# Kernel tuning notes

Hardware: AMD Instinct MI355X
Metric: run time of the kernel (lower is better)

Reference implementation:

```python
import jax, jax.numpy as jnp
import numpy as np

DN = ('NCHW', 'OIHW', 'NCHW')
B, H, W = 2048, 16, 16
DICT, SE, CE, ESZ, NZ = 14, 8, 16, 512, 512
EPS = 1e-4


def _conv(x, w, b):
    # 3x3 conv, padding=1 (SAME), NCHW
    return jax.lax.conv_general_dilated(x, w, (1, 1), 'SAME', dimension_numbers=DN) + b[None, :, None, None]


def _normalized(m, eps=0.0):
    return m / (jnp.sqrt(jnp.sum(m * m, axis=1, keepdims=True)) + eps)


def setup_inputs() -> dict:
    key = jax.random.key(0)
    ks = jax.random.split(key, 20)
    f = jnp.float32
    d = {
        's': jax.random.randint(ks[0], (B, H, W), 0, DICT, dtype=jnp.int32),
        's_prime': jax.random.randint(ks[1], (B, H, W), 0, DICT, dtype=jnp.int32),
        'state_embed': jax.random.normal(ks[2], (DICT, SE), f),
        'conv_embed_w': jax.random.normal(ks[3], (CE, SE, 3, 3), f) * 0.1,
        'conv_embed_b': jnp.zeros((CE,), f),
        'p1c1_w': jax.random.normal(ks[4], (16, CE, 3, 3), f) * 0.1,
        'p1c1_b': jnp.zeros((16,), f),
        'p1c2_w': jax.random.normal(ks[5], (32, 16, 3, 3), f) * 0.1,
        'p1c2_b': jnp.zeros((32,), f),
        'p1l_w': jax.random.normal(ks[6], (ESZ, 32 * H * W), f) * 0.02,
        'p1l_b': jnp.zeros((ESZ,), f),
        'p2c1_w': jax.random.normal(ks[7], (16, CE, 3, 3), f) * 0.1,
        'p2c1_b': jnp.zeros((16,), f),
        'p2c2_w': jax.random.normal(ks[8], (32, 16, 3, 3), f) * 0.1,
        'p2c2_b': jnp.zeros((32,), f),
        'p2l_w': jax.random.normal(ks[9], (ESZ, 32 * H * W), f) * 0.02,
        'p2l_b': jnp.zeros((ESZ,), f),
        'z_vectors': jax.random.normal(ks[10], (NZ, ESZ), f),
        'scale': jnp.ones((1,), f),
        'downscale_factor': 1,
    }
    return d


def _embed(s, state_embed, conv_embed_w, conv_embed_b):
    # nn.Embedding(max_norm=1): renorm rows to L2 norm <= 1 before lookup
    norms = jnp.sqrt(jnp.sum(state_embed * state_embed, axis=1, keepdims=True))
    table = state_embed / jnp.maximum(norms, 1.0)
    x = table[s]  # (B, H, W, SE)
    x = jnp.transpose(x, (0, 3, 1, 2))  # (B, SE, H, W)
    return _conv(x, conv_embed_w, conv_embed_b)


def _tower(x, c1w, c1b, c2w, c2b, lw, lb):
    x = jax.nn.relu(_conv(x, c1w, c1b))
    x = jax.nn.relu(_conv(x, c2w, c2b))
    x = x.reshape(x.shape[0], -1)  # (B, 32*H*W)
    x = x @ lw.T + lb
    return _normalized(x, EPS)


def reference(s, s_prime, state_embed, conv_embed_w, conv_embed_b,
              p1c1_w, p1c1_b, p1c2_w, p1c2_b, p1l_w, p1l_b,
              p2c1_w, p2c1_b, p2c2_w, p2c2_b, p2l_w, p2l_b,
              z_vectors, scale, downscale_factor):
    s_e = _embed(s, state_embed, conv_embed_w, conv_embed_b)
    sp_e = _embed(s_prime, state_embed, conv_embed_w, conv_embed_b)
    embed1 = _tower(s_e, p1c1_w, p1c1_b, p1c2_w, p1c2_b, p1l_w, p1l_b)
    embed2 = _tower(sp_e - s_e, p2c1_w, p2c1_b, p2c2_w, p2c2_b, p2l_w, p2l_b)
    # VQ: cosine-similarity nearest codebook vector
    zn = _normalized(z_vectors, 0.0)  # (NZ, ESZ)
    z_inds = jnp.argmax(embed2 @ zn.T, axis=1)  # (B,)
    z_matrix = zn[z_inds]  # (B, ESZ)
    if downscale_factor == 1:
        ipm = embed1 @ z_matrix.T  # (B, B)
    else:
        bs = embed1.shape[0] // downscale_factor
        v1 = embed1[::downscale_factor]  # (bs, ESZ)
        v2 = z_matrix.reshape(bs, downscale_factor, -1)
        ipm = jnp.einsum('be,bde->bd', v1, v2)
    return jnp.exp(scale) * ipm
```

## Files before the change

### kernel.cpp

```cpp
#include <hip/hip_runtime.h>
#include <math.h>


typedef __attribute__((ext_vector_type(8))) __bf16 bf16x8;
typedef __attribute__((ext_vector_type(4))) float f32x4;
typedef __attribute__((ext_vector_type(8))) unsigned short ushort8;
typedef __attribute__((ext_vector_type(4))) unsigned short ushort4v;

static __device__ __forceinline__ unsigned short f2bf(float x) {
  union { float f; unsigned u; } v; v.f = x;
  return (unsigned short)(v.u >> 16);
}
static __device__ __forceinline__ float bf2f(unsigned short h) {
  union { float f; unsigned u; } v; v.u = ((unsigned)h) << 16;
  return v.f;
}
template<int NS>
static __device__ __forceinline__ void split3(float x, unsigned short* h) {
  unsigned short q0 = f2bf(x); h[0] = q0;
  float r1 = x - bf2f(q0);
  unsigned short q1 = f2bf(r1); h[1] = q1;
  if constexpr (NS == 3) h[2] = f2bf(r1 - bf2f(q1));
}
static __device__ __forceinline__ void gload_lds16(const void* g, void* l) {
  __builtin_amdgcn_global_load_lds(
      (const __attribute__((address_space(1))) unsigned int*)g,
      (__attribute__((address_space(3))) unsigned int*)l, 16, 0, 0);
}
#define MFMA16(a, b, c) __builtin_amdgcn_mfma_f32_16x16x32_bf16((a), (b), (c), 0, 0, 0)

template<int NS>
static __device__ __forceinline__ f32x4 mfma_prod(const bf16x8* a, const bf16x8* b, f32x4 c) {
  c = MFMA16(a[0], b[0], c);
  c = MFMA16(a[0], b[1], c);
  c = MFMA16(a[1], b[0], c);
  if constexpr (NS == 3) {
    c = MFMA16(a[1], b[1], c);
    c = MFMA16(a[0], b[2], c);
    c = MFMA16(a[2], b[0], c);
  }
  return c;
}
static __device__ __forceinline__ int conv_a16(int cell, int half) {
  return (cell * 2 + half) ^ ((cell >> 2) & 7);
}

__global__ __launch_bounds__(128) void prep_table_kernel(
    const float* __restrict__ se, float* __restrict__ tbl)
{
  int t = threadIdx.x;
  if (t < 112) {
    int r = t >> 3;
    float ss = 0.f;
    #pragma unroll
    for (int i = 0; i < 8; ++i) { float v = se[r * 8 + i]; ss += v * v; }
    float n = fmaxf(sqrtf(ss), 1.0f);
    tbl[t] = se[t] / n;
  }
}

__global__ __launch_bounds__(256) void reduce_norm_kernel(
    const float* __restrict__ pre, const float* __restrict__ bias, float eps,
    unsigned short* __restrict__ o0, unsigned short* __restrict__ o1,
    unsigned short* __restrict__ o2)
{
  int row = blockIdx.x, t = threadIdx.x;
  size_t base = (size_t)row * 512 + t * 2;
  float2 v = *reinterpret_cast<const float2*>(pre + base);
  float ax = v.x, ay = v.y;
  if (bias) { ax += bias[t * 2]; ay += bias[t * 2 + 1]; }
  float ss = ax * ax + ay * ay;
  #pragma unroll
  for (int m = 32; m >= 1; m >>= 1) ss += __shfl_xor(ss, m, 64);
  __shared__ float wsum[4];
  int lane = t & 63, wid = t >> 6;
  if (lane == 0) wsum[wid] = ss;
  __syncthreads();
  float tot = wsum[0] + wsum[1] + wsum[2] + wsum[3];
  float inv = 1.0f / (sqrtf(tot) + eps);
  float a = ax * inv, b = ay * inv;
  unsigned short ha[3], hb[3];
  split3<3>(a, ha); split3<3>(b, hb);
  o0[base] = ha[0]; o0[base + 1] = hb[0];
  o1[base] = ha[1]; o1[base + 1] = hb[1];
  if (o2) { o2[base] = ha[2]; o2[base + 1] = hb[2]; }
}

__global__ __launch_bounds__(256) void prep_wt_kernel(
    const float* __restrict__ src, unsigned short* __restrict__ dst,
    int NSs, int OC, int mode)
{
  int total = 3 * NSs * 4 * OC * 8;
  int i = blockIdx.x * 256 + threadIdx.x;
  if (i >= total) return;
  int ic = i & 7;
  int r = i >> 3;
  int oc = r % OC; r /= OC;
  int kc = r & 3; r >>= 2;
  int s = r % NSs;
  int sp = r / NSs;
  int tap, icf, IC;
  if (mode == 0) { tap = s * 4 + kc; icf = ic; IC = 8; }
  else           { tap = s * 2 + (kc >> 1); icf = (kc & 1) * 8 + ic; IC = 16; }
  float w = 0.f;
  if (tap < 9) {
    int ky = tap / 3, kx = tap - ky * 3;
    w = src[((oc * IC + icf) * 3 + ky) * 3 + kx];
  }
  unsigned short h[3];
  split3<3>(w, h);
  dst[i] = h[sp];
}

template<int NS>
__global__ __launch_bounds__(256) void tower_mfma_kernel(
    const int* __restrict__ sIdx, const int* __restrict__ spIdx,
    const float* __restrict__ tblf,
    const unsigned short* __restrict__ wtE,
    const unsigned short* __restrict__ wt1,
    const unsigned short* __restrict__ wt2,
    const float* __restrict__ eb, const float* __restrict__ c1b,
    const float* __restrict__ c2b,
    unsigned short* __restrict__ a0, unsigned short* __restrict__ a1,
    unsigned short* __restrict__ a2, int delta)
{
  __shared__ float tbl[112];
  __shared__ ushort8 G[NS][324];
  __shared__ ushort8 Abuf[NS][648];
  __shared__ ushort8 Bbuf[NS][648];

  const int b = blockIdx.x, t = threadIdx.x;
  const int lane = t & 63, wv = t >> 6;
  const int fr = lane & 15, kc = lane >> 4;

  if (t < 112) tbl[t] = tblf[t];
  {
    int4 zz = {0, 0, 0, 0};
    int4* gz = (int4*)G;
    for (int i = t; i < NS * 324; i += 256) gz[i] = zz;
    int4* az = (int4*)Abuf;
    for (int i = t; i < NS * 648; i += 256) az[i] = zz;
    int4* bz = (int4*)Bbuf;
    for (int i = t; i < NS * 648; i += 256) bz[i] = zz;
  }
  __syncthreads();

  {
    const int y = t >> 4, x = t & 15;
    const int cell = (y + 1) * 18 + (x + 1);
    int sv = sIdx[(size_t)b * 256 + t];
    float v[8];
    if (delta) {
      int spv = spIdx[(size_t)b * 256 + t];
      #pragma unroll
      for (int c = 0; c < 8; ++c) v[c] = tbl[spv * 8 + c] - tbl[sv * 8 + c];
    } else {
      #pragma unroll
      for (int c = 0; c < 8; ++c) v[c] = tbl[sv * 8 + c];
    }
    ushort8 h0, h1, h2;
    #pragma unroll
    for (int c = 0; c < 8; ++c) {
      unsigned short q[3];
      split3<NS>(v[c], q);
      h0[c] = q[0]; h1[c] = q[1];
      if constexpr (NS == 3) h2[c] = q[2];
    }
    G[0][cell] = h0; G[1][cell] = h1;
    if constexpr (NS == 3) G[2][cell] = h2;
  }
  __syncthreads();

  {
    float bias = 0.f;
    if (!delta) bias = eb[fr];
    f32x4 acc[4];
    #pragma unroll
    for (int j = 0; j < 4; ++j) acc[j] = (f32x4)0.f;
    #pragma unroll
    for (int s = 0; s < 3; ++s) {
      bf16x8 bw[NS];
      #pragma unroll
      for (int sp = 0; sp < NS; ++sp)
        bw[sp] = __builtin_bit_cast(bf16x8, *reinterpret_cast<const ushort8*>(
            wtE + (size_t)(((sp * 3 + s) * 4 + kc) * 16 + fr) * 8));
      int tap = s * 4 + kc; if (tap > 8) tap = 8;
      const int dy = tap / 3, dx = tap - dy * 3;
      const int cb = dy * 18 + fr + dx;
      #pragma unroll
      for (int j = 0; j < 4; ++j) {
        const int cell = cb + (wv * 4 + j) * 18;
        bf16x8 av[NS];
        #pragma unroll
        for (int sp = 0; sp < NS; ++sp)
          av[sp] = __builtin_bit_cast(bf16x8, G[sp][cell]);
        acc[j] = mfma_prod<NS>(av, bw, acc[j]);
      }
    }
    #pragma unroll
    for (int j = 0; j < 4; ++j) {
      const int y = wv * 4 + j;
      #pragma unroll
      for (int q = 0; q < 4; ++q) {
        const int x = kc * 4 + q;
        const int cell = (y + 1) * 18 + (x + 1);
        const int a16 = conv_a16(cell, fr >> 3);
        unsigned short hh[3];
        split3<NS>(acc[j][q] + bias, hh);
        #pragma unroll
        for (int sp = 0; sp < NS; ++sp)
          ((unsigned short*)&Abuf[sp][0])[a16 * 8 + (fr & 7)] = hh[sp];
      }
    }
  }
  __syncthreads();

  {
    const float bias = c1b[fr];
    f32x4 acc[4];
    #pragma unroll
    for (int j = 0; j < 4; ++j) acc[j] = (f32x4)0.f;
    #pragma unroll
    for (int s = 0; s < 5; ++s) {
      bf16x8 bw[NS];
      #pragma unroll
      for (int sp = 0; sp < NS; ++sp)
        bw[sp] = __builtin_bit_cast(bf16x8, *reinterpret_cast<const ushort8*>(
            wt1 + (size_t)(((sp * 5 + s) * 4 + kc) * 16 + fr) * 8));
      int tap = s * 2 + (kc >> 1); if (tap > 8) tap = 8;
      const int dy = tap / 3, dx = tap - dy * 3;
      const int half = kc & 1;
      const int cb = dy * 18 + fr + dx;
      #pragma unroll
      for (int j = 0; j < 4; ++j) {
        const int cell = cb + (wv * 4 + j) * 18;
        const int a16 = conv_a16(cell, half);
        bf16x8 av[NS];
        #pragma unroll
        for (int sp = 0; sp < NS; ++sp)
          av[sp] = __builtin_bit_cast(bf16x8, *reinterpret_cast<const ushort8*>(
              (const unsigned short*)&Abuf[sp][0] + a16 * 8));
        acc[j] = mfma_prod<NS>(av, bw, acc[j]);
      }
    }
    #pragma unroll
    for (int j = 0; j < 4; ++j) {
      const int y = wv * 4 + j;
      #pragma unroll
      for (int q = 0; q < 4; ++q) {
        const int x = kc * 4 + q;
        const int cell = (y + 1) * 18 + (x + 1);
        const int a16 = conv_a16(cell, fr >> 3);
        unsigned short hh[3];
        split3<NS>(fmaxf(acc[j][q] + bias, 0.f), hh);
        #pragma unroll
        for (int sp = 0; sp < NS; ++sp)
          ((unsigned short*)&Bbuf[sp][0])[a16 * 8 + (fr & 7)] = hh[sp];
      }
    }
  }
  __syncthreads();

  {
    const float bias0 = c2b[fr], bias1 = c2b[16 + fr];
    f32x4 acc0[4], acc1[4];
    #pragma unroll
    for (int j = 0; j < 4; ++j) { acc0[j] = (f32x4)0.f; acc1[j] = (f32x4)0.f; }
    #pragma unroll
    for (int s = 0; s < 5; ++s) {
      bf16x8 bw0[NS], bw1[NS];
      #pragma unroll
      for (int sp = 0; sp < NS; ++sp) {
        size_t base = (size_t)(((sp * 5 + s) * 4 + kc) * 32) * 8;
        bw0[sp] = __builtin_bit_cast(bf16x8,
            *reinterpret_cast<const ushort8*>(wt2 + base + (size_t)fr * 8));
        bw1[sp] = __builtin_bit_cast(bf16x8,
            *reinterpret_cast<const ushort8*>(wt2 + base + (size_t)(16 + fr) * 8));
      }
      int tap = s * 2 + (kc >> 1); if (tap > 8) tap = 8;
      const int dy = tap / 3, dx = tap - dy * 3;
      const int half = kc & 1;
      const int cb = dy * 18 + fr + dx;
      #pragma unroll
      for (int j = 0; j < 4; ++j) {
        const int cell = cb + (wv * 4 + j) * 18;
        const int a16 = conv_a16(cell, half);
        bf16x8 av[NS];
        #pragma unroll
        for (int sp = 0; sp < NS; ++sp)
          av[sp] = __builtin_bit_cast(bf16x8, *reinterpret_cast<const ushort8*>(
              (const unsigned short*)&Bbuf[sp][0] + a16 * 8));
        acc0[j] = mfma_prod<NS>(av, bw0, acc0[j]);
        acc1[j] = mfma_prod<NS>(av, bw1, acc1[j]);
      }
    }
    #pragma unroll
    for (int j = 0; j < 4; ++j) {
      const int y = wv * 4 + j;
      ushort4v g0[2], g1[2], g2[2];
      #pragma unroll
      for (int q = 0; q < 4; ++q) {
        unsigned short hh[3];
        split3<NS>(fmaxf(acc0[j][q] + bias0, 0.f), hh);
        g0[0][q] = hh[0]; g1[0][q] = hh[1]; if constexpr (NS == 3) g2[0][q] = hh[2];
        split3<NS>(fmaxf(acc1[j][q] + bias1, 0.f), hh);
        g0[1][q] = hh[0]; g1[1][q] = hh[1]; if constexpr (NS == 3) g2[1][q] = hh[2];
      }
      size_t base0 = (size_t)b * 8192 + (size_t)fr * 256 + y * 16 + kc * 4;
      size_t base1 = base0 + 16 * 256;
      *reinterpret_cast<ushort4v*>(a0 + base0) = g0[0];
      *reinterpret_cast<ushort4v*>(a0 + base1) = g0[1];
      *reinterpret_cast<ushort4v*>(a1 + base0) = g1[0];
      *reinterpret_cast<ushort4v*>(a1 + base1) = g1[1];
      if constexpr (NS == 3) {
        *reinterpret_cast<ushort4v*>(a2 + base0) = g2[0];
        *reinterpret_cast<ushort4v*>(a2 + base1) = g2[1];
      }
    }
  }
}

template<int NS, bool BF32, bool GATHER, bool ATOMIC, bool FINAL>
__global__ __launch_bounds__(256) void mfma_gemm_kernel(
    const unsigned short* __restrict__ A0, const unsigned short* __restrict__ A1,
    const unsigned short* __restrict__ A2,
    const unsigned short* __restrict__ B0, const unsigned short* __restrict__ B1,
    const unsigned short* __restrict__ B2,
    const float* __restrict__ Bf32,
    const int* __restrict__ gather, const float* __restrict__ scale_p,
    float* __restrict__ C, int M, int N, int K, int Ksub)
{
  __shared__ unsigned short ldsA[NS][4096];
  __shared__ unsigned short ldsB[NS][4096];

  const int t = threadIdx.x;
  const int lane = t & 63, wv = t >> 6;
  const int m0 = blockIdx.x * 128, n0 = blockIdx.y * 128;
  const long kbase = (long)blockIdx.z * Ksub;
  const int NT = Ksub >> 5;

  const int st_row = lane >> 2;
  const int st_cb = (lane & 3) * 16;
  int srow[2];
  long bgrow[2];
  #pragma unroll
  for (int r = 0; r < 2; ++r) {
    srow[r] = (wv + 4 * r) * 16 + st_row;
    if constexpr (!BF32) {
      long g = n0 + srow[r];
      if constexpr (GATHER) g = gather[n0 + srow[r]];
      bgrow[r] = g;
    }
  }

  const int wr = wv >> 1, wc = wv & 1;
  const int fr = lane & 15, kc = lane >> 4;

  f32x4 acc[4][4];
  #pragma unroll
  for (int mi = 0; mi < 4; ++mi)
    #pragma unroll
    for (int ni = 0; ni < 4; ++ni) acc[mi][ni] = (f32x4)0.f;

  const unsigned short* Asp[3] = {A0, A1, A2};
  const unsigned short* Bsp[3] = {B0, B1, B2};

  for (int kt = 0; kt < NT; ++kt) {
    const long k0 = kbase + (long)kt * 32;
    #pragma unroll
    for (int sp = 0; sp < NS; ++sp)
      #pragma unroll
      for (int r = 0; r < 2; ++r) {
        int row = srow[r];
        int c = st_cb ^ (((row >> 1) & 3) << 4);
        gload_lds16(Asp[sp] + (size_t)(m0 + row) * K + k0 + (c >> 1),
                    &ldsA[sp][(wv + 4 * r) * 512]);
      }
    if constexpr (BF32) {
      #pragma unroll
      for (int i = 0; i < 4; ++i) {
        int row = (t >> 3) + 32 * i;
        f32x4 v = *reinterpret_cast<const f32x4*>(
            Bf32 + (size_t)(n0 + row) * K + k0 + (t & 7) * 4);
        int cb = ((t & 7) * 8) ^ (((row >> 1) & 3) << 4);
        ushort4v w0, w1, w2;
        #pragma unroll
        for (int jj = 0; jj < 4; ++jj) {
          unsigned short hh[3];
          split3<NS>(v[jj], hh);
          w0[jj] = hh[0]; w1[jj] = hh[1];
          if constexpr (NS == 3) w2[jj] = hh[2];
        }
        *reinterpret_cast<ushort4v*>(&ldsB[0][row * 32 + (cb >> 1)]) = w0;
        *reinterpret_cast<ushort4v*>(&ldsB[1][row * 32 + (cb >> 1)]) = w1;
        if constexpr (NS == 3)
          *reinterpret_cast<ushort4v*>(&ldsB[2][row * 32 + (cb >> 1)]) = w2;
      }
    } else {
      #pragma unroll
      for (int sp = 0; sp < NS; ++sp)
        #pragma unroll
        for (int r = 0; r < 2; ++r) {
          int row = srow[r];
          int c = st_cb ^ (((row >> 1) & 3) << 4);
          gload_lds16(Bsp[sp] + (size_t)bgrow[r] * K + k0 + (c >> 1),
                      &ldsB[sp][(wv + 4 * r) * 512]);
        }
    }
    __syncthreads();

    bf16x8 af[NS][4], bf[NS][4];
    #pragma unroll
    for (int sp = 0; sp < NS; ++sp) {
      #pragma unroll
      for (int mi = 0; mi < 4; ++mi) {
        int row = wr * 64 + mi * 16 + fr;
        int cb = (kc * 16) ^ (((row >> 1) & 3) << 4);
        af[sp][mi] = __builtin_bit_cast(bf16x8,
            *reinterpret_cast<const ushort8*>(&ldsA[sp][row * 32 + (cb >> 1)]));
      }
      #pragma unroll
      for (int ni = 0; ni < 4; ++ni) {
        int row = wc * 64 + ni * 16 + fr;
        int cb = (kc * 16) ^ (((row >> 1) & 3) << 4);
        bf[sp][ni] = __builtin_bit_cast(bf16x8,
            *reinterpret_cast<const ushort8*>(&ldsB[sp][row * 32 + (cb >> 1)]));
      }
    }
    #pragma unroll
    for (int mi = 0; mi < 4; ++mi)
      #pragma unroll
      for (int ni = 0; ni < 4; ++ni) {
        f32x4 c = acc[mi][ni];
        c = MFMA16(af[0][mi], bf[0][ni], c);
        c = MFMA16(af[0][mi], bf[1][ni], c);
        c = MFMA16(af[1][mi], bf[0][ni], c);
        if constexpr (NS == 3) {
          c = MFMA16(af[1][mi], bf[1][ni], c);
          c = MFMA16(af[0][mi], bf[2][ni], c);
          c = MFMA16(af[2][mi], bf[0][ni], c);
        }
        acc[mi][ni] = c;
      }
    __syncthreads();
  }

  if constexpr (ATOMIC) {
    #pragma unroll
    for (int mi = 0; mi < 4; ++mi)
      #pragma unroll
      for (int ni = 0; ni < 4; ++ni) {
        int col = n0 + wc * 64 + ni * 16 + fr;
        #pragma unroll
        for (int q = 0; q < 4; ++q) {
          int row = m0 + wr * 64 + mi * 16 + kc * 4 + q;
          atomicAdd(&C[(size_t)row * N + col], acc[mi][ni][q]);
        }
      }
  } else {
    float scl = 1.0f;
    if constexpr (FINAL) scl = expf(scale_p[0]);
    #pragma unroll
    for (int mi = 0; mi < 4; ++mi)
      #pragma unroll
      for (int ni = 0; ni < 4; ++ni) {
        int col = n0 + wc * 64 + ni * 16 + fr;
        #pragma unroll
        for (int q = 0; q < 4; ++q) {
          int row = m0 + wr * 64 + mi * 16 + kc * 4 + q;
          C[(size_t)row * N + col] = acc[mi][ni][q] * scl;
        }
      }
  }
}

__global__ __launch_bounds__(256) void argmax_rows_kernel(
    const float* __restrict__ S, int* __restrict__ inds)
{
  __shared__ float vals[256];
  __shared__ int idxs[256];
  int row = blockIdx.x, t = threadIdx.x;
  float best = -INFINITY; int bi = 1 << 30;
  #pragma unroll
  for (int r = 0; r < 2; ++r) {
    int j = t + r * 256;
    float v = S[(size_t)row * 512 + j];
    if (v > best) { best = v; bi = j; }
  }
  vals[t] = best; idxs[t] = bi;
  __syncthreads();
  for (int off = 128; off > 0; off >>= 1) {
    if (t < off) {
      float v2 = vals[t + off]; int i2 = idxs[t + off];
      if (v2 > vals[t] || (v2 == vals[t] && i2 < idxs[t])) {
        vals[t] = v2; idxs[t] = i2;
      }
    }
    __syncthreads();
  }
  if (t == 0) inds[row] = idxs[0];
}

extern "C" void kernel_launch(void* const* d_in, const int* in_sizes, int n_in,
                              void* d_out, int out_size, void* d_ws, size_t ws_size,
                              hipStream_t stream)
{
  const int*   s      = (const int*)  d_in[0];
  const int*   sprime = (const int*)  d_in[1];
  const float* se     = (const float*)d_in[2];
  const float* ew     = (const float*)d_in[3];
  const float* eb     = (const float*)d_in[4];
  const float* p1c1w  = (const float*)d_in[5];
  const float* p1c1b  = (const float*)d_in[6];
  const float* p1c2w  = (const float*)d_in[7];
  const float* p1c2b  = (const float*)d_in[8];
  const float* p1lw   = (const float*)d_in[9];
  const float* p1lb   = (const float*)d_in[10];
  const float* p2c1w  = (const float*)d_in[11];
  const float* p2c1b  = (const float*)d_in[12];
  const float* p2c2w  = (const float*)d_in[13];
  const float* p2c2b  = (const float*)d_in[14];
  const float* p2lw   = (const float*)d_in[15];
  const float* p2lb   = (const float*)d_in[16];
  const float* zv     = (const float*)d_in[17];
  const float* scale  = (const float*)d_in[18];
  float* out = (float*)d_out;

  char* w = (char*)d_ws;
  size_t off = 0;
  auto alloc = [&](size_t bytes) -> char* {
    char* p = w + off;
    off += (bytes + 255) & ~(size_t)255;
    return p;
  };
  float* tblf = (float*)alloc(112 * 4);
  unsigned short* zn0 = (unsigned short*)alloc((size_t)512 * 512 * 2);
  unsigned short* zn1 = (unsigned short*)alloc((size_t)512 * 512 * 2);
  unsigned short* zn2 = (unsigned short*)alloc((size_t)512 * 512 * 2);
  unsigned short* e10 = (unsigned short*)alloc((size_t)2048 * 512 * 2);
  unsigned short* e11 = (unsigned short*)alloc((size_t)2048 * 512 * 2);
  unsigned short* e20 = (unsigned short*)alloc((size_t)2048 * 512 * 2);
  unsigned short* e21 = (unsigned short*)alloc((size_t)2048 * 512 * 2);
  unsigned short* e22 = (unsigned short*)alloc((size_t)2048 * 512 * 2);
  float* epre = (float*)alloc((size_t)2048 * 512 * 4);
  float* sc   = epre;
  int*   zi   = (int*)alloc(2048 * 4);
  unsigned short* wtE  = (unsigned short*)alloc(4608 * 2);
  unsigned short* wt1a = (unsigned short*)alloc(7680 * 2);
  unsigned short* wt2a = (unsigned short*)alloc(15360 * 2);
  unsigned short* wt1b = (unsigned short*)alloc(7680 * 2);
  unsigned short* wt2b = (unsigned short*)alloc(15360 * 2);
  unsigned short* act0 = (unsigned short*)alloc((size_t)2048 * 8192 * 2);
  unsigned short* act1 = (unsigned short*)alloc((size_t)2048 * 8192 * 2);
  unsigned short* act2 = (unsigned short*)alloc((size_t)2048 * 8192 * 2);

  prep_table_kernel<<<1, 128, 0, stream>>>(se, tblf);
  reduce_norm_kernel<<<512, 256, 0, stream>>>(zv, nullptr, 0.0f, zn0, zn1, zn2);
  prep_wt_kernel<<<18, 256, 0, stream>>>(ew,    wtE,  3, 16, 0);
  prep_wt_kernel<<<30, 256, 0, stream>>>(p1c1w, wt1a, 5, 16, 1);
  prep_wt_kernel<<<60, 256, 0, stream>>>(p1c2w, wt2a, 5, 32, 1);
  prep_wt_kernel<<<30, 256, 0, stream>>>(p2c1w, wt1b, 5, 16, 1);
  prep_wt_kernel<<<60, 256, 0, stream>>>(p2c2w, wt2b, 5, 32, 1);

  tower_mfma_kernel<2><<<2048, 256, 0, stream>>>(
      s, sprime, tblf, wtE, wt1a, wt2a, eb, p1c1b, p1c2b, act0, act1, act2, 0);
  hipMemsetAsync(epre, 0, (size_t)2048 * 512 * 4, stream);
  mfma_gemm_kernel<2, true, false, true, false><<<dim3(16, 4, 8), 256, 0, stream>>>(
      act0, act1, nullptr, nullptr, nullptr, nullptr, p1lw, nullptr, nullptr,
      epre, 2048, 512, 8192, 1024);
  reduce_norm_kernel<<<2048, 256, 0, stream>>>(epre, p1lb, 1e-4f, e10, e11, nullptr);

  tower_mfma_kernel<3><<<2048, 256, 0, stream>>>(
      s, sprime, tblf, wtE, wt1b, wt2b, eb, p2c1b, p2c2b, act0, act1, act2, 1);
  hipMemsetAsync(epre, 0, (size_t)2048 * 512 * 4, stream);
  mfma_gemm_kernel<3, true, false, true, false><<<dim3(16, 4, 8), 256, 0, stream>>>(
      act0, act1, act2, nullptr, nullptr, nullptr, p2lw, nullptr, nullptr,
      epre, 2048, 512, 8192, 1024);
  reduce_norm_kernel<<<2048, 256, 0, stream>>>(epre, p2lb, 1e-4f, e20, e21, e22);

  mfma_gemm_kernel<3, false, false, false, false><<<dim3(16, 4, 1), 256, 0, stream>>>(
      e20, e21, e22, zn0, zn1, zn2, nullptr, nullptr, nullptr,
      sc, 2048, 512, 512, 512);
  argmax_rows_kernel<<<2048, 256, 0, stream>>>(sc, zi);
  mfma_gemm_kernel<2, false, true, false, true><<<dim3(16, 16, 1), 256, 0, stream>>>(
      e10, e11, nullptr, zn0, zn1, nullptr, nullptr, zi, scale,
      out, 2048, 2048, 512, 512);
}
```

Measured before the change: 486.4 us.

## Fuse argmax into score GEMM, merge prep kernels, trim halo zeroing, deepen split-K

New measurement: 502.7 us. 1.03x slower.

```diff
diff --git a/kernel.cpp b/kernel.cpp
--- a/kernel.cpp
+++ b/kernel.cpp
@@ -44,55 +44,79 @@
 static __device__ __forceinline__ int conv_a16(int cell, int half) {
   return (cell * 2 + half) ^ ((cell >> 2) & 7);
 }
-
-__global__ __launch_bounds__(128) void prep_table_kernel(
-    const float* __restrict__ se, float* __restrict__ tbl)
+static __device__ __forceinline__ unsigned long long score_key(float v, int col) {
+  unsigned b = __float_as_uint(v);
+  unsigned m = b ^ ((unsigned)((int)b >> 31) | 0x80000000u);
+  return ((unsigned long long)m << 32) | (unsigned)(511 - col);
+}
+static __device__ __forceinline__ unsigned long long shfl_xor_u64(unsigned long long v, int m) {
+  unsigned lo = __shfl_xor((unsigned)v, m, 64);
+  unsigned hi = __shfl_xor((unsigned)(v >> 32), m, 64);
+  return ((unsigned long long)hi << 32) | lo;
+}
+
+__global__ __launch_bounds__(256) void prep_misc_kernel(
+    const float* __restrict__ se, float* __restrict__ tbl,
+    const float* __restrict__ zv,
+    unsigned short* __restrict__ zn0, unsigned short* __restrict__ zn1,
+    unsigned short* __restrict__ zn2,
+    float* __restrict__ epre, unsigned long long* __restrict__ zi)
 {
-  int t = threadIdx.x;
-  if (t < 112) {
-    int r = t >> 3;
-    float ss = 0.f;
-    #pragma unroll
-    for (int i = 0; i < 8; ++i) { float v = se[r * 8 + i]; ss += v * v; }
-    float n = fmaxf(sqrtf(ss), 1.0f);
-    tbl[t] = se[t] / n;
-  }
-}
-
-__global__ __launch_bounds__(256) void reduce_norm_kernel(
-    const float* __restrict__ pre, const float* __restrict__ bias, float eps,
-    unsigned short* __restrict__ o0, unsigned short* __restrict__ o1,
-    unsigned short* __restrict__ o2)
+  __shared__ float wsum[4];
+  const int b = blockIdx.x, t = threadIdx.x;
+  if (b == 0) {
+    if (t < 112) {
+      int r = t >> 3;
+      float ss = 0.f;
+      #pragma unroll
+      for (int i = 0; i < 8; ++i) { float v = se[r * 8 + i]; ss += v * v; }
+      float n = fmaxf(sqrtf(ss), 1.0f);
+      tbl[t] = se[t] / n;
+    }
+  } else if (b <= 512) {
+    int row = b - 1;
+    size_t base = (size_t)row * 512 + t * 2;
+    float2 v = *reinterpret_cast<const float2*>(zv + base);
+    float ss = v.x * v.x + v.y * v.y;
+    #pragma unroll
+    for (int m = 32; m >= 1; m >>= 1) ss += __shfl_xor(ss, m, 64);
+    int lane = t & 63, wid = t >> 6;
+    if (lane == 0) wsum[wid] = ss;
+    __syncthreads();
+    float tot = wsum[0] + wsum[1] + wsum[2] + wsum[3];
+    float inv = 1.0f / sqrtf(tot);
+    float a = v.x * inv, c = v.y * inv;
+    unsigned short ha[3], hc[3];
+    split3<3>(a, ha); split3<3>(c, hc);
+    zn0[base] = ha[0]; zn0[base + 1] = hc[0];
+    zn1[base] = ha[1]; zn1[base + 1] = hc[1];
+    zn2[base] = ha[2]; zn2[base + 1] = hc[2];
+  } else if (b <= 1024) {
+    f32x4 z4 = {0.f, 0.f, 0.f, 0.f};
+    size_t o = ((size_t)(b - 513) * 256 + t) * 8;
+    *reinterpret_cast<f32x4*>(epre + o) = z4;
+    *reinterpret_cast<f32x4*>(epre + o + 4) = z4;
+  } else {
+    int i = (b - 1025) * 256 + t;
+    if (i < 2048) zi[i] = 0ull;
+  }
+}
+
+__global__ __launch_bounds__(256) void prep_wt_all_kernel(
+    const float* __restrict__ ew,
+    const float* __restrict__ p1c1w, const float* __restrict__ p1c2w,
+    const float* __restrict__ p2c1w, const float* __restrict__ p2c2w,
+    unsigned short* __restrict__ wt)
 {
-  int row = blockIdx.x, t = threadIdx.x;
-  size_t base = (size_t)row * 512 + t * 2;
-  float2 v = *reinterpret_cast<const float2*>(pre + base);
-  float ax = v.x, ay = v.y;
-  if (bias) { ax += bias[t * 2]; ay += bias[t * 2 + 1]; }
-  float ss = ax * ax + ay * ay;
-  #pragma unroll
-  for (int m = 32; m >= 1; m >>= 1) ss += __shfl_xor(ss, m, 64);
-  __shared__ float wsum[4];
-  int lane = t & 63, wid = t >> 6;
-  if (lane == 0) wsum[wid] = ss;
-  __syncthreads();
-  float tot = wsum[0] + wsum[1] + wsum[2] + wsum[3];
-  float inv = 1.0f / (sqrtf(tot) + eps);
-  float a = ax * inv, b = ay * inv;
-  unsigned short ha[3], hb[3];
-  split3<3>(a, ha); split3<3>(b, hb);
-  o0[base] = ha[0]; o0[base + 1] = hb[0];
-  o1[base] = ha[1]; o1[base + 1] = hb[1];
-  if (o2) { o2[base] = ha[2]; o2[base + 1] = hb[2]; }
-}
-
-__global__ __launch_bounds__(256) void prep_wt_kernel(
-    const float* __restrict__ src, unsigned short* __restrict__ dst,
-    int NSs, int OC, int mode)
-{
-  int total = 3 * NSs * 4 * OC * 8;
-  int i = blockIdx.x * 256 + threadIdx.x;
-  if (i >= total) return;
+  int gi = blockIdx.x * 256 + threadIdx.x;
+  if (gi >= 50688) return;
+  const float* src; int off, NSs, OC, mode;
+  if (gi < 4608)       { src = ew;    off = 0;     NSs = 3; OC = 16; mode = 0; }
+  else if (gi < 12288) { src = p1c1w; off = 4608;  NSs = 5; OC = 16; mode = 1; }
+  else if (gi < 27648) { src = p1c2w; off = 12288; NSs = 5; OC = 32; mode = 1; }
+  else if (gi < 35328) { src = p2c1w; off = 27648; NSs = 5; OC = 16; mode = 1; }
+  else                 { src = p2c2w; off = 35328; NSs = 5; OC = 32; mode = 1; }
+  int i = gi - off;
   int ic = i & 7;
   int r = i >> 3;
   int oc = r % OC; r /= OC;
@@ -109,7 +133,37 @@
   }
   unsigned short h[3];
   split3<3>(w, h);
-  dst[i] = h[sp];
+  wt[gi] = h[sp];
+}
+
+__global__ __launch_bounds__(256) void reduce_norm_kernel(
+    const float* __restrict__ pre, const float* __restrict__ bias, float eps,
+    unsigned short* __restrict__ o0, unsigned short* __restrict__ o1,
+    unsigned short* __restrict__ o2, float* __restrict__ zero_dst)
+{
+  int row = blockIdx.x, t = threadIdx.x;
+  size_t base = (size_t)row * 512 + t * 2;
+  float2 v = *reinterpret_cast<const float2*>(pre + base);
+  float ax = v.x + bias[t * 2], ay = v.y + bias[t * 2 + 1];
+  float ss = ax * ax + ay * ay;
+  #pragma unroll
+  for (int m = 32; m >= 1; m >>= 1) ss += __shfl_xor(ss, m, 64);
+  __shared__ float wsum[4];
+  int lane = t & 63, wid = t >> 6;
+  if (lane == 0) wsum[wid] = ss;
+  __syncthreads();
+  float tot = wsum[0] + wsum[1] + wsum[2] + wsum[3];
+  float inv = 1.0f / (sqrtf(tot) + eps);
+  float a = ax * inv, b2 = ay * inv;
+  unsigned short ha[3], hb[3];
+  split3<3>(a, ha); split3<3>(b2, hb);
+  o0[base] = ha[0]; o0[base + 1] = hb[0];
+  o1[base] = ha[1]; o1[base + 1] = hb[1];
+  if (o2) { o2[base] = ha[2]; o2[base + 1] = hb[2]; }
+  if (zero_dst) {
+    float2 z = {0.f, 0.f};
+    *reinterpret_cast<float2*>(zero_dst + base) = z;
+  }
 }
 
 template<int NS>
@@ -134,14 +188,21 @@
   const int fr = lane & 15, kc = lane >> 4;
 
   if (t < 112) tbl[t] = tblf[t];
-  {
-    int4 zz = {0, 0, 0, 0};
-    int4* gz = (int4*)G;
-    for (int i = t; i < NS * 324; i += 256) gz[i] = zz;
-    int4* az = (int4*)Abuf;
-    for (int i = t; i < NS * 648; i += 256) az[i] = zz;
-    int4* bz = (int4*)Bbuf;
-    for (int i = t; i < NS * 648; i += 256) bz[i] = zz;
+  if (t < 68) {
+    int c;
+    if (t < 18)      c = t;
+    else if (t < 36) c = 306 + (t - 18);
+    else if (t < 52) c = 18 * (t - 35);
+    else             c = 18 * (t - 51) + 17;
+    ushort8 z8 = {0, 0, 0, 0, 0, 0, 0, 0};
+    #pragma unroll
+    for (int sp = 0; sp < NS; ++sp) {
+      G[sp][c] = z8;
+      ((ushort8*)&Abuf[sp][0])[conv_a16(c, 0)] = z8;
+      ((ushort8*)&Abuf[sp][0])[conv_a16(c, 1)] = z8;
+      ((ushort8*)&Bbuf[sp][0])[conv_a16(c, 0)] = z8;
+      ((ushort8*)&Bbuf[sp][0])[conv_a16(c, 1)] = z8;
+    }
   }
   __syncthreads();
 
@@ -320,14 +381,16 @@
   }
 }
 
-template<int NS, bool BF32, bool GATHER, bool ATOMIC, bool FINAL>
+template<int NS, bool BF32, int EPI>
 __global__ __launch_bounds__(256) void mfma_gemm_kernel(
     const unsigned short* __restrict__ A0, const unsigned short* __restrict__ A1,
     const unsigned short* __restrict__ A2,
     const unsigned short* __restrict__ B0, const unsigned short* __restrict__ B1,
     const unsigned short* __restrict__ B2,
     const float* __restrict__ Bf32,
-    const int* __restrict__ gather, const float* __restrict__ scale_p,
+    const unsigned long long* __restrict__ gkey,
+    unsigned long long* __restrict__ zout,
+    const float* __restrict__ scale_p,
     float* __restrict__ C, int M, int N, int K, int Ksub)
 {
   __shared__ unsigned short ldsA[NS][4096];
@@ -348,7 +411,8 @@
     srow[r] = (wv + 4 * r) * 16 + st_row;
     if constexpr (!BF32) {
       long g = n0 + srow[r];
-      if constexpr (GATHER) g = gather[n0 + srow[r]];
+      if constexpr (EPI == 2)
+        g = 511 - (long)(unsigned)(gkey[n0 + srow[r]] & 0xFFFFFFFFull);
       bgrow[r] = g;
     }
   }
@@ -445,7 +509,7 @@
     __syncthreads();
   }
 
-  if constexpr (ATOMIC) {
+  if constexpr (EPI == 0) {
     #pragma unroll
     for (int mi = 0; mi < 4; ++mi)
       #pragma unroll
@@ -457,9 +521,8 @@
           atomicAdd(&C[(size_t)row * N + col], acc[mi][ni][q]);
         }
       }
-  } else {
-    float scl = 1.0f;
-    if constexpr (FINAL) scl = expf(scale_p[0]);
+  } else if constexpr (EPI == 2) {
+    float scl = expf(scale_p[0]);
     #pragma unroll
     for (int mi = 0; mi < 4; ++mi)
       #pragma unroll
@@ -471,34 +534,27 @@
           C[(size_t)row * N + col] = acc[mi][ni][q] * scl;
         }
       }
-  }
-}
-
-__global__ __launch_bounds__(256) void argmax_rows_kernel(
-    const float* __restrict__ S, int* __restrict__ inds)
-{
-  __shared__ float vals[256];
-  __shared__ int idxs[256];
-  int row = blockIdx.x, t = threadIdx.x;
-  float best = -INFINITY; int bi = 1 << 30;
-  #pragma unroll
-  for (int r = 0; r < 2; ++r) {
-    int j = t + r * 256;
-    float v = S[(size_t)row * 512 + j];
-    if (v > best) { best = v; bi = j; }
-  }
-  vals[t] = best; idxs[t] = bi;
-  __syncthreads();
-  for (int off = 128; off > 0; off >>= 1) {
-    if (t < off) {
-      float v2 = vals[t + off]; int i2 = idxs[t + off];
-      if (v2 > vals[t] || (v2 == vals[t] && i2 < idxs[t])) {
-        vals[t] = v2; idxs[t] = i2;
-      }
-    }
-    __syncthreads();
-  }
-  if (t == 0) inds[row] = idxs[0];
+  } else {
+    #pragma unroll
+    for (int mi = 0; mi < 4; ++mi)
+      #pragma unroll
+      for (int q = 0; q < 4; ++q) {
+        int row = m0 + wr * 64 + mi * 16 + kc * 4 + q;
+        unsigned long long best = 0ull;
+        #pragma unroll
+        for (int ni = 0; ni < 4; ++ni) {
+          int col = n0 + wc * 64 + ni * 16 + fr;
+          unsigned long long k2 = score_key(acc[mi][ni][q], col);
+          best = (k2 > best) ? k2 : best;
+        }
+        #pragma unroll
+        for (int m2 = 1; m2 < 16; m2 <<= 1) {
+          unsigned long long o = shfl_xor_u64(best, m2);
+          best = (o > best) ? o : best;
+        }
+        if (fr == 0) atomicMax(zout + row, best);
+      }
+  }
 }
 
 extern "C" void kernel_launch(void* const* d_in, const int* in_sizes, int n_in,
@@ -543,46 +599,41 @@
   unsigned short* e21 = (unsigned short*)alloc((size_t)2048 * 512 * 2);
   unsigned short* e22 = (unsigned short*)alloc((size_t)2048 * 512 * 2);
   float* epre = (float*)alloc((size_t)2048 * 512 * 4);
-  float* sc   = epre;
-  int*   zi   = (int*)alloc(2048 * 4);
-  unsigned short* wtE  = (unsigned short*)alloc(4608 * 2);
-  unsigned short* wt1a = (unsigned short*)alloc(7680 * 2);
-  unsigned short* wt2a = (unsigned short*)alloc(15360 * 2);
-  unsigned short* wt1b = (unsigned short*)alloc(7680 * 2);
-  unsigned short* wt2b = (unsigned short*)alloc(15360 * 2);
+  unsigned long long* zi = (unsigned long long*)alloc(2048 * 8);
+  unsigned short* wt = (unsigned short*)alloc((size_t)50688 * 2);
   unsigned short* act0 = (unsigned short*)alloc((size_t)2048 * 8192 * 2);
   unsigned short* act1 = (unsigned short*)alloc((size_t)2048 * 8192 * 2);
   unsigned short* act2 = (unsigned short*)alloc((size_t)2048 * 8192 * 2);
 
-  prep_table_kernel<<<1, 128, 0, stream>>>(se, tblf);
-  reduce_norm_kernel<<<512, 256, 0, stream>>>(zv, nullptr, 0.0f, zn0, zn1, zn2);
-  prep_wt_kernel<<<18, 256, 0, stream>>>(ew,    wtE,  3, 16, 0);
-  prep_wt_kernel<<<30, 256, 0, stream>>>(p1c1w, wt1a, 5, 16, 1);
-  prep_wt_kernel<<<60, 256, 0, stream>>>(p1c2w, wt2a, 5, 32, 1);
-  prep_wt_kernel<<<30, 256, 0, stream>>>(p2c1w, wt1b, 5, 16, 1);
-  prep_wt_kernel<<<60, 256, 0, stream>>>(p2c2w, wt2b, 5, 32, 1);
+  unsigned short* wtE  = wt;
+  unsigned short* wt1a = wt + 4608;
+  unsigned short* wt2a = wt + 12288;
+  unsigned short* wt1b = wt + 27648;
+  unsigned short* wt2b = wt + 35328;
+
+  prep_misc_kernel<<<1033, 256, 0, stream>>>(se, tblf, zv, zn0, zn1, zn2, epre, zi);
+  prep_wt_all_kernel<<<198, 256, 0, stream>>>(ew, p1c1w, p1c2w, p2c1w, p2c2w, wt);
 
   tower_mfma_kernel<2><<<2048, 256, 0, stream>>>(
       s, sprime, tblf, wtE, wt1a, wt2a, eb, p1c1b, p1c2b, act0, act1, act2, 0);
-  hipMemsetAsync(epre, 0, (size_t)2048 * 512 * 4, stream);
-  mfma_gemm_kernel<2, true, false, true, false><<<dim3(16, 4, 8), 256, 0, stream>>>(
+  mfma_gemm_kernel<2, true, 0><<<dim3(16, 4, 16), 256, 0, stream>>>(
       act0, act1, nullptr, nullptr, nullptr, nullptr, p1lw, nullptr, nullptr,
-      epre, 2048, 512, 8192, 1024);
-  reduce_norm_kernel<<<2048, 256, 0, stream>>>(epre, p1lb, 1e-4f, e10, e11, nullptr);
+      nullptr, epre, 2048, 512, 8192, 512);
+  reduce_norm_kernel<<<2048, 256, 0, stream>>>(epre, p1lb, 1e-4f,
+                                               e10, e11, nullptr, epre);
 
   tower_mfma_kernel<3><<<2048, 256, 0, stream>>>(
       s, sprime, tblf, wtE, wt1b, wt2b, eb, p2c1b, p2c2b, act0, act1, act2, 1);
-  hipMemsetAsync(epre, 0, (size_t)2048 * 512 * 4, stream);
-  mfma_gemm_kernel<3, true, false, true, false><<<dim3(16, 4, 8), 256, 0, stream>>>(
+  mfma_gemm_kernel<3, true, 0><<<dim3(16, 4, 16), 256, 0, stream>>>(
       act0, act1, act2, nullptr, nullptr, nullptr, p2lw, nullptr, nullptr,
-      epre, 2048, 512, 8192, 1024);
-  reduce_norm_kernel<<<2048, 256, 0, stream>>>(epre, p2lb, 1e-4f, e20, e21, e22);
-
-  mfma_gemm_kernel<3, false, false, false, false><<<dim3(16, 4, 1), 256, 0, stream>>>(
-      e20, e21, e22, zn0, zn1, zn2, nullptr, nullptr, nullptr,
-      sc, 2048, 512, 512, 512);
-  argmax_rows_kernel<<<2048, 256, 0, stream>>>(sc, zi);
-  mfma_gemm_kernel<2, false, true, false, true><<<dim3(16, 16, 1), 256, 0, stream>>>(
-      e10, e11, nullptr, zn0, zn1, nullptr, nullptr, zi, scale,
+      nullptr, epre, 2048, 512, 8192, 512);
+  reduce_norm_kernel<<<2048, 256, 0, stream>>>(epre, p2lb, 1e-4f,
+                                               e20, e21, e22, nullptr);
+
+  mfma_gemm_kernel<3, false, 3><<<dim3(16, 4, 1), 256, 0, stream>>>(
+      e20, e21, e22, zn0, zn1, zn2, nullptr, nullptr, zi, nullptr,
+      nullptr, 2048, 512, 512, 512);
+  mfma_gemm_kernel<2, false, 2><<<dim3(16, 16, 1), 256, 0, stream>>>(
+      e10, e11, nullptr, zn0, zn1, nullptr, nullptr, zi, nullptr, scale,
       out, 2048, 2048, 512, 512);
 }
```
